# Optimization experiments

Hardware: AMD Instinct MI355X
Metric: run time of the kernel (lower is better)

## Reference

```python
import jax, jax.numpy as jnp
import numpy as np

NUM_NODES = 100000
HIDDEN = 128
NUM_EDGES = 625000


def setup_inputs() -> dict:
    key = jax.random.key(0)
    k_emb, k_edge = jax.random.split(key)
    node_ids = jnp.arange(NUM_NODES, dtype=jnp.int64 if jax.config.jax_enable_x64 else jnp.int32)
    edge_index = jax.random.randint(k_edge, (2, NUM_EDGES), 0, NUM_NODES, dtype=jnp.int32)
    emb_weight = jax.random.normal(k_emb, (NUM_NODES, HIDDEN), dtype=jnp.float32)
    return {"node_ids": node_ids, "edge_index": edge_index, "emb_weight": emb_weight}


def reference(node_ids, edge_index, emb_weight):
    # sources = node_ids[edge_index[0]]; vs = emb[sources]  -> [E, H] gather
    sources = node_ids[edge_index[0]]
    vs = emb_weight[sources]  # [E, H]
    tgt = edge_index[1]
    # scatter_mean over dim 0: segment-sum then divide by per-target counts
    sums = jax.ops.segment_sum(vs, tgt, num_segments=NUM_NODES)  # [N, H]
    counts = jax.ops.segment_sum(jnp.ones((vs.shape[0],), dtype=vs.dtype), tgt,
                                 num_segments=NUM_NODES)  # [N]
    # empty segments -> 0 (matches torch_scatter scatter_mean)
    return sums / jnp.maximum(counts, 1.0)[:, None]
```

## Files before the change

kernel.cpp:

```cpp
#include <hip/hip_runtime.h>


#define NUM_NODES 100000
#define HIDDEN    128
#define NUM_EDGES 625000
#define CAP       32

#define EDGE_PER_THREAD 8
#define EDGE_THREADS (NUM_EDGES / EDGE_PER_THREAD)
#define EDGE_BLOCKS  ((EDGE_THREADS + 255) / 256)
#define CAST_THREADS (NUM_NODES * HIDDEN / 16)
#define CAST_BLOCKS  (CAST_THREADS / 256)
#define PREP_BLOCKS  (EDGE_BLOCKS + CAST_BLOCKS)

typedef float vfloat4 __attribute__((ext_vector_type(4)));

__device__ __forceinline__ unsigned bf16_rne(float f) {
    unsigned x = __float_as_uint(f);
    return (x + 0x7FFFu + ((x >> 16) & 1u)) >> 16;
}

__device__ __forceinline__ unsigned pack2(float lo, float hi) {
    return bf16_rne(lo) | (bf16_rne(hi) << 16);
}

__global__ __launch_bounds__(256) void prep_kernel(
    const int* __restrict__ node_ids,
    const int* __restrict__ src,
    const int* __restrict__ tgt,
    const float* __restrict__ emb,
    int* __restrict__ cnt,
    int* __restrict__ buckets,
    uint4* __restrict__ emb16)
{
    int bid = blockIdx.x;
    int tid = threadIdx.x;

    if (bid < EDGE_BLOCKS) {
        int et = bid * 256 + tid;
        if (et >= EDGE_THREADS) return;
        int e0 = et * EDGE_PER_THREAD;
        int4 sa = *reinterpret_cast<const int4*>(src + e0);
        int4 sb = *reinterpret_cast<const int4*>(src + e0 + 4);
        int4 ta = *reinterpret_cast<const int4*>(tgt + e0);
        int4 tb = *reinterpret_cast<const int4*>(tgt + e0 + 4);

        int n0 = node_ids[sa.x], n1 = node_ids[sa.y];
        int n2 = node_ids[sa.z], n3 = node_ids[sa.w];
        int n4 = node_ids[sb.x], n5 = node_ids[sb.y];
        int n6 = node_ids[sb.z], n7 = node_ids[sb.w];

        int p0 = atomicAdd(&cnt[ta.x], 1);
        int p1 = atomicAdd(&cnt[ta.y], 1);
        int p2 = atomicAdd(&cnt[ta.z], 1);
        int p3 = atomicAdd(&cnt[ta.w], 1);
        int p4 = atomicAdd(&cnt[tb.x], 1);
        int p5 = atomicAdd(&cnt[tb.y], 1);
        int p6 = atomicAdd(&cnt[tb.z], 1);
        int p7 = atomicAdd(&cnt[tb.w], 1);

        if (p0 < CAP) buckets[ta.x * CAP + p0] = n0;
        if (p1 < CAP) buckets[ta.y * CAP + p1] = n1;
        if (p2 < CAP) buckets[ta.z * CAP + p2] = n2;
        if (p3 < CAP) buckets[ta.w * CAP + p3] = n3;
        if (p4 < CAP) buckets[tb.x * CAP + p4] = n4;
        if (p5 < CAP) buckets[tb.y * CAP + p5] = n5;
        if (p6 < CAP) buckets[tb.z * CAP + p6] = n6;
        if (p7 < CAP) buckets[tb.w * CAP + p7] = n7;
    } else {
        int j = (bid - EDGE_BLOCKS) * 256 + tid;
        const float4* ev = reinterpret_cast<const float4*>(emb);
        float4 a = ev[j * 4 + 0];
        float4 b = ev[j * 4 + 1];
        float4 c = ev[j * 4 + 2];
        float4 d = ev[j * 4 + 3];
        uint4 o0, o1;
        o0.x = pack2(a.x, a.y); o0.y = pack2(a.z, a.w);
        o0.z = pack2(b.x, b.y); o0.w = pack2(b.z, b.w);
        o1.x = pack2(c.x, c.y); o1.y = pack2(c.z, c.w);
        o1.z = pack2(d.x, d.y); o1.w = pack2(d.z, d.w);
        emb16[j * 2 + 0] = o0;
        emb16[j * 2 + 1] = o1;
    }
}

__global__ __launch_bounds__(256) void gather_kernel(
    const int* __restrict__ cnt, const int* __restrict__ buckets,
    const uint4* __restrict__ emb16, float* __restrict__ out)
{
    int gid  = blockIdx.x * blockDim.x + threadIdx.x;
    int n    = gid >> 4;
    int lane = gid & 15;
    if (n >= NUM_NODES) return;

    int c = cnt[n];
    int m = (c < CAP) ? c : CAP;
    const int* b = buckets + n * CAP;

    float acc[8] = {0,0,0,0,0,0,0,0};

    auto accum = [&](uint4 u) {
        acc[0] += __uint_as_float(u.x << 16);
        acc[1] += __uint_as_float(u.x & 0xFFFF0000u);
        acc[2] += __uint_as_float(u.y << 16);
        acc[3] += __uint_as_float(u.y & 0xFFFF0000u);
        acc[4] += __uint_as_float(u.z << 16);
        acc[5] += __uint_as_float(u.z & 0xFFFF0000u);
        acc[6] += __uint_as_float(u.w << 16);
        acc[7] += __uint_as_float(u.w & 0xFFFF0000u);
    };

    int i = 0;
    for (; i + 3 < m; i += 4) {
        int4 s = *reinterpret_cast<const int4*>(b + i);
        uint4 u0 = emb16[(size_t)s.x * 16 + lane];
        uint4 u1 = emb16[(size_t)s.y * 16 + lane];
        uint4 u2 = emb16[(size_t)s.z * 16 + lane];
        uint4 u3 = emb16[(size_t)s.w * 16 + lane];
        accum(u0); accum(u1); accum(u2); accum(u3);
    }
    for (; i < m; ++i) {
        uint4 u = emb16[(size_t)b[i] * 16 + lane];
        accum(u);
    }

    float inv = (c > 0) ? 1.0f / (float)c : 0.0f;
    vfloat4 r0, r1;
    r0.x = acc[0] * inv; r0.y = acc[1] * inv; r0.z = acc[2] * inv; r0.w = acc[3] * inv;
    r1.x = acc[4] * inv; r1.y = acc[5] * inv; r1.z = acc[6] * inv; r1.w = acc[7] * inv;
    float* o = out + (size_t)n * HIDDEN + lane * 8;
    __builtin_nontemporal_store(r0, reinterpret_cast<vfloat4*>(o));
    __builtin_nontemporal_store(r1, reinterpret_cast<vfloat4*>(o + 4));
}

extern "C" void kernel_launch(void* const* d_in, const int* in_sizes, int n_in,
                              void* d_out, int out_size, void* d_ws, size_t ws_size,
                              hipStream_t stream) {
    const int*   node_ids = (const int*)d_in[0];
    const int*   edge_idx = (const int*)d_in[1];
    const float* emb      = (const float*)d_in[2];
    float*       out      = (float*)d_out;

    const int* edge_src = edge_idx;
    const int* edge_tgt = edge_idx + NUM_EDGES;

    char* ws = (char*)d_ws;
    int*   cnt     = (int*)(ws + 0);
    int*   buckets = (int*)(ws + 400000);
    uint4* emb16   = (uint4*)(ws + 13200000);

    (void)hipMemsetAsync(cnt, 0, NUM_NODES * sizeof(int), stream);

    prep_kernel<<<PREP_BLOCKS, 256, 0, stream>>>(node_ids, edge_src, edge_tgt,
                                                 emb, cnt, buckets, emb16);
    {
        long long total = (long long)NUM_NODES * 16;
        int grid = (int)((total + 255) / 256);
        gather_kernel<<<grid, 256, 0, stream>>>(cnt, buckets, emb16, out);
    }
}
```

Baseline: 171.4 us.

## Interleave edge bucketing and bf16 cast within every prep block

Replaces the split prep grid, where some blocks did edge bucketing and the others did the embedding cast, with a uniform grid. Each block now handles 200 edges (one per thread) and also casts its 256-row slice of the embedding. Atomic latency and scattered bucket stores can then overlap with the streaming embedding loads in the same wave. The cost is lower edge work per thread (1 instead of 8) and 56 idle edge lanes per block.

```diff
diff --git a/kernel.cpp b/kernel.cpp
--- a/kernel.cpp
+++ b/kernel.cpp
@@ -6,12 +6,8 @@
 #define NUM_EDGES 625000
 #define CAP       32
 
-#define EDGE_PER_THREAD 8
-#define EDGE_THREADS (NUM_EDGES / EDGE_PER_THREAD)
-#define EDGE_BLOCKS  ((EDGE_THREADS + 255) / 256)
-#define CAST_THREADS (NUM_NODES * HIDDEN / 16)
-#define CAST_BLOCKS  (CAST_THREADS / 256)
-#define PREP_BLOCKS  (EDGE_BLOCKS + CAST_BLOCKS)
+#define PREP_BLOCKS 3125
+#define EDGES_PER_BLOCK 200
 
 typedef float vfloat4 __attribute__((ext_vector_type(4)));
 
@@ -36,52 +32,33 @@
     int bid = blockIdx.x;
     int tid = threadIdx.x;
 
-    if (bid < EDGE_BLOCKS) {
-        int et = bid * 256 + tid;
-        if (et >= EDGE_THREADS) return;
-        int e0 = et * EDGE_PER_THREAD;
-        int4 sa = *reinterpret_cast<const int4*>(src + e0);
-        int4 sb = *reinterpret_cast<const int4*>(src + e0 + 4);
-        int4 ta = *reinterpret_cast<const int4*>(tgt + e0);
-        int4 tb = *reinterpret_cast<const int4*>(tgt + e0 + 4);
+    int t = -1, nid = 0;
+    if (tid < EDGES_PER_BLOCK) {
+        int e = bid * EDGES_PER_BLOCK + tid;
+        t   = tgt[e];
+        nid = node_ids[src[e]];
+    }
 
-        int n0 = node_ids[sa.x], n1 = node_ids[sa.y];
-        int n2 = node_ids[sa.z], n3 = node_ids[sa.w];
-        int n4 = node_ids[sb.x], n5 = node_ids[sb.y];
-        int n6 = node_ids[sb.z], n7 = node_ids[sb.w];
+    int j = bid * 256 + tid;
+    const float4* ev = reinterpret_cast<const float4*>(emb);
+    float4 a = ev[j * 4 + 0];
+    float4 b = ev[j * 4 + 1];
+    float4 c = ev[j * 4 + 2];
+    float4 d = ev[j * 4 + 3];
 
-        int p0 = atomicAdd(&cnt[ta.x], 1);
-        int p1 = atomicAdd(&cnt[ta.y], 1);
-        int p2 = atomicAdd(&cnt[ta.z], 1);
-        int p3 = atomicAdd(&cnt[ta.w], 1);
-        int p4 = atomicAdd(&cnt[tb.x], 1);
-        int p5 = atomicAdd(&cnt[tb.y], 1);
-        int p6 = atomicAdd(&cnt[tb.z], 1);
-        int p7 = atomicAdd(&cnt[tb.w], 1);
+    int pos = 0;
+    if (t >= 0) pos = atomicAdd(&cnt[t], 1);
 
-        if (p0 < CAP) buckets[ta.x * CAP + p0] = n0;
-        if (p1 < CAP) buckets[ta.y * CAP + p1] = n1;
-        if (p2 < CAP) buckets[ta.z * CAP + p2] = n2;
-        if (p3 < CAP) buckets[ta.w * CAP + p3] = n3;
-        if (p4 < CAP) buckets[tb.x * CAP + p4] = n4;
-        if (p5 < CAP) buckets[tb.y * CAP + p5] = n5;
-        if (p6 < CAP) buckets[tb.z * CAP + p6] = n6;
-        if (p7 < CAP) buckets[tb.w * CAP + p7] = n7;
-    } else {
-        int j = (bid - EDGE_BLOCKS) * 256 + tid;
-        const float4* ev = reinterpret_cast<const float4*>(emb);
-        float4 a = ev[j * 4 + 0];
-        float4 b = ev[j * 4 + 1];
-        float4 c = ev[j * 4 + 2];
-        float4 d = ev[j * 4 + 3];
-        uint4 o0, o1;
-        o0.x = pack2(a.x, a.y); o0.y = pack2(a.z, a.w);
-        o0.z = pack2(b.x, b.y); o0.w = pack2(b.z, b.w);
-        o1.x = pack2(c.x, c.y); o1.y = pack2(c.z, c.w);
-        o1.z = pack2(d.x, d.y); o1.w = pack2(d.z, d.w);
-        emb16[j * 2 + 0] = o0;
-        emb16[j * 2 + 1] = o1;
-    }
+    uint4 o0, o1;
+    o0.x = pack2(a.x, a.y); o0.y = pack2(a.z, a.w);
+    o0.z = pack2(b.x, b.y); o0.w = pack2(b.z, b.w);
+    o1.x = pack2(c.x, c.y); o1.y = pack2(c.z, c.w);
+    o1.z = pack2(d.x, d.y); o1.w = pack2(d.z, d.w);
+    emb16[j * 2 + 0] = o0;
+    emb16[j * 2 + 1] = o1;
+
+    if (t >= 0 && pos < CAP)
+        buckets[t * CAP + pos] = nid;
 }
 
 __global__ __launch_bounds__(256) void gather_kernel(
```

Result: faster. 166.9 us (-2.6%).
